# Kernel tuning notes

Hardware: AMD Instinct MI355X
Metric: run time of the kernel (lower is better)

Reference implementation:

```python
import jax, jax.numpy as jnp
import numpy as np

K = 8           # neighbor_num
H = 8           # n_heads
DH = 64         # dim_single_head


def setup_inputs() -> dict:
    key = jax.random.key(0)
    ks = jax.random.split(key, 6)
    B, N, D = 2, 8192, 256
    inner = H * DH  # 512
    x = jax.random.normal(ks[0], (B, N, D), jnp.float32)
    center_pos3d = jax.random.normal(ks[1], (B, N, 3), jnp.float32)
    Wq = jax.random.normal(ks[2], (D, inner), jnp.float32) * 0.02
    Wkv = jax.random.normal(ks[3], (D, 2 * inner), jnp.float32) * 0.02
    Wout = jax.random.normal(ks[4], (inner, D), jnp.float32) * 0.02
    bout = jnp.zeros((D,), jnp.float32)
    return {"x": x, "center_pos3d": center_pos3d, "Wq": Wq, "Wkv": Wkv,
            "Wout": Wout, "bout": bout}


def _knn_idx(pos, k):
    # pos: [B,N,3] -> indices of k nearest neighbors per point, [B,N,k]
    sq = jnp.sum(pos * pos, axis=-1)                      # [B,N]
    d2 = sq[:, :, None] + sq[:, None, :] - 2.0 * jnp.einsum('bnc,bmc->bnm', pos, pos)
    _, idx = jax.lax.top_k(-d2, k)                        # smallest distances
    return idx


def reference(x, center_pos3d, Wq, Wkv, Wout, bout):
    B, N, D = x.shape
    inner = H * DH
    scale = DH ** -0.5

    idx = _knn_idx(center_pos3d, K)                       # [B,N,K] int32
    # grouping_operation: gather neighbor features -> [B,N,K,D]
    knn_x = jax.vmap(lambda xb, ib: xb[ib])(x, idx)

    q = (x @ Wq).reshape(B, N, H, DH)                     # [B,N,H,DH]
    kv = knn_x @ Wkv                                      # [B,N,K,2*inner]
    k_, v_ = jnp.split(kv, 2, axis=-1)
    k_ = k_.reshape(B, N, K, H, DH)
    v_ = v_.reshape(B, N, K, H, DH)

    dots = jnp.einsum('bnhd,bnkhd->bnhk', q, k_) * scale  # [B,N,H,K]
    attn = jax.nn.softmax(dots, axis=-1)
    out = jnp.einsum('bnhk,bnkhd->bnhd', attn, v_)        # [B,N,H,DH]
    out = out.reshape(B, N, inner)
    return out @ Wout + bout                              # dropout p=0 -> identity
```

## Files before the change

### kernel.cpp

```cpp
#include <hip/hip_runtime.h>
#include <hip/hip_bf16.h>

#define N_PTS 8192
#define KNN 8

typedef __attribute__((ext_vector_type(8))) short short8;
typedef __attribute__((ext_vector_type(4))) float float4v;
typedef unsigned long long u64;

static __device__ __forceinline__ short f2bf(float f) {
    unsigned u = __float_as_uint(f);
    unsigned r = (u + 0x7FFFu + ((u >> 16) & 1u)) >> 16;
    return (short)r;
}
static __device__ __forceinline__ float bf2f(short s) {
    return __uint_as_float(((unsigned)(unsigned short)s) << 16);
}

static __device__ __forceinline__ unsigned sortkey(float f) {
    unsigned u = __float_as_uint(f);
    return u ^ (((unsigned)((int)u >> 31)) | 0x80000000u);
}

static __device__ __forceinline__ void ins8(u64* best, u64 x) {
#pragma unroll
    for (int j = 0; j < 8; ++j) {
        const u64 lo = x < best[j] ? x : best[j];
        const u64 hi = x < best[j] ? best[j] : x;
        best[j] = lo; x = hi;
    }
}

static __device__ __forceinline__ void vmin_acc(float& acc, float d) {
    asm("v_min_f32 %0, %0, %1" : "+v"(acc) : "v"(d));
}
static __device__ __forceinline__ void vsort2(float& a, float& x) {
    float lo, hi;
    asm("v_min_f32 %0, %2, %3\n\tv_max_f32 %1, %2, %3"
        : "=&v"(lo), "=v"(hi) : "v"(a), "v"(x));
    a = lo; x = hi;
}

__global__ __launch_bounds__(256) void fused_knn_conv(const float* __restrict__ pos,
                                                      u64* __restrict__ partial,
                                                      const float* __restrict__ x,
                                                      const float* __restrict__ Wq,
                                                      const float* __restrict__ Wkv,
                                                      const float* __restrict__ Wout,
                                                      short* __restrict__ xb,
                                                      short* __restrict__ wqkvt,
                                                      short* __restrict__ woutt)
{
    __shared__ __align__(16) char smem[16896];
    const int tid = threadIdx.x;
    const int g5 = blockIdx.x / 5;
    const int r5 = blockIdx.x % 5;

    if (r5 == 0) {
        const int kb = g5;
        float4* cand = (float4*)smem;
        unsigned short* buf = (unsigned short*)(smem + 8192);

        const int p   = kb & 15;
        const int qg  = kb >> 4;
        const int batch = qg >> 5;
        const int q_in_b = (qg & 31) * 256 + tid;
        const float* bpos = pos + (long)batch * N_PTS * 3;

        if (tid < 128) {
            const float* src = bpos + (p * 512 + tid * 4) * 3;
            const float4 f0 = *(const float4*)(src);
            const float4 f1 = *(const float4*)(src + 4);
            const float4 f2 = *(const float4*)(src + 8);
            const int c0 = tid * 4;
            cand[c0 + 0] = make_float4(f0.x, f0.y, f0.z,
                                       fmaf(f0.x, f0.x, fmaf(f0.y, f0.y, f0.z * f0.z)));
            cand[c0 + 1] = make_float4(f0.w, f1.x, f1.y,
                                       fmaf(f0.w, f0.w, fmaf(f1.x, f1.x, f1.y * f1.y)));
            cand[c0 + 2] = make_float4(f1.z, f1.w, f2.x,
                                       fmaf(f1.z, f1.z, fmaf(f1.w, f1.w, f2.x * f2.x)));
            cand[c0 + 3] = make_float4(f2.y, f2.z, f2.w,
                                       fmaf(f2.y, f2.y, fmaf(f2.z, f2.z, f2.w * f2.w)));
        }
        __syncthreads();

        const float qx = bpos[q_in_b * 3 + 0];
        const float qy = bpos[q_in_b * 3 + 1];
        const float qz = bpos[q_in_b * 3 + 2];
        const float nqx = -2.0f * qx;
        const float nqy = -2.0f * qy;
        const float nqz = -2.0f * qz;

        float bmin[32];
#pragma unroll
        for (int j = 0; j < 32; ++j) bmin[j] = 3.0e38f;

        for (int base = 0; base < 512; base += 32) {
#pragma unroll
            for (int g = 0; g < 32; ++g) {
                const float4 c = cand[base + g];
                const float d = fmaf(c.x, nqx, fmaf(c.y, nqy, fmaf(c.z, nqz, c.w)));
                vmin_acc(bmin[g], d);
            }
        }

        float t8[8];
#pragma unroll
        for (int j = 0; j < 8; ++j) t8[j] = 3.0e38f;
#pragma unroll
        for (int i = 0; i < 32; ++i) {
            float x_ = bmin[i];
#pragma unroll
            for (int j = 0; j < 8; ++j)
                vsort2(t8[j], x_);
        }
        const float t = t8[7];

        int cnt = 0;
        for (int base = 0; base < 512; base += 32) {
#pragma unroll
            for (int g = 0; g < 32; ++g) {
                const float4 c = cand[base + g];
                const float d = fmaf(c.x, nqx, fmaf(c.y, nqy, fmaf(c.z, nqz, c.w)));
                if (d <= t) {
                    buf[tid * 17 + (cnt < 16 ? cnt : 16)] = (unsigned short)(base + g);
                    ++cnt;
                }
            }
        }

        u64 best[8];
#pragma unroll
        for (int j = 0; j < 8; ++j) best[j] = ~0ULL;

        if (cnt <= 16) {
            for (int u = 0; u < cnt; ++u) {
                const int i = buf[tid * 17 + u];
                const float4 c = cand[i];
                const float d = fmaf(c.x, nqx, fmaf(c.y, nqy, fmaf(c.z, nqz, c.w)));
                ins8(best, ((u64)sortkey(d) << 32) | (unsigned)(p * 512 + i));
            }
        } else {
            for (int i = 0; i < 512; ++i) {
                const float4 c = cand[i];
                const float d = fmaf(c.x, nqx, fmaf(c.y, nqy, fmaf(c.z, nqz, c.w)));
                const u64 x_ = ((u64)sortkey(d) << 32) | (unsigned)(p * 512 + i);
                if (x_ < best[7]) ins8(best, x_);
            }
        }

        const long qglob = (long)batch * N_PTS + q_in_b;
#pragma unroll
        for (int j = 0; j < 8; ++j)
            partial[(long)(p * 8 + j) * 16384 + qglob] = best[j];

    } else {
        const int bid = g5 * 4 + (r5 - 1);
        if (bid < 2048) {
            const int i = bid * 256 + tid;
            const float4 a = ((const float4*)x)[i * 2];
            const float4 b = ((const float4*)x)[i * 2 + 1];
            short8 w = {f2bf(a.x), f2bf(a.y), f2bf(a.z), f2bf(a.w),
                        f2bf(b.x), f2bf(b.y), f2bf(b.z), f2bf(b.w)};
            ((short8*)xb)[i] = w;
        } else if (bid < 2560) {
            const int o = (bid - 2048) * 256 + tid;
            const int n = o >> 8, k = o & 255;
            wqkvt[o] = f2bf(Wq[(long)k * 512 + n]);
        } else if (bid < 3584) {
            const int o = (bid - 2560) * 256 + tid;
            const int n = o >> 8, k = o & 255;
            wqkvt[131072 + o] = f2bf(Wkv[(long)k * 1024 + n]);
        } else {
            const int o = (bid - 3584) * 256 + tid;
            const int n = o >> 9, k = o & 511;
            woutt[o] = f2bf(Wout[(long)k * 256 + n]);
        }
    }
}

__global__ __launch_bounds__(256) void fused_gemm_merge(const short* __restrict__ A,
                                                        const short* __restrict__ Bt,
                                                        short* __restrict__ qall,
                                                        short* __restrict__ kvall,
                                                        const u64* __restrict__ partial,
                                                        int* __restrict__ idxo)
{
    __shared__ short As[128][40];
    __shared__ short Bs[128][40];

    const int tid = threadIdx.x;

    if (blockIdx.x < 64) {
        const int q = blockIdx.x * 256 + tid;
        u64 best[8];
#pragma unroll
        for (int j = 0; j < 8; ++j) best[j] = ~0ULL;
        for (int s = 0; s < 128; ++s) {
            u64 x = partial[(long)s * 16384 + q];
            if (x < best[7]) ins8(best, x);
        }
#pragma unroll
        for (int j = 0; j < 8; ++j)
            idxo[(long)q * 8 + j] = (int)(best[j] & 0xFFFFFFFFu);
        return;
    }

    const int id = blockIdx.x - 64;
    const int bx = id % 12;
    const int by = id / 12;

    const int lane = tid & 63;
    const int wv   = tid >> 6;
    const int quad = lane >> 4;
    const int l15  = lane & 15;
    const int m0 = by * 128;
    const int n0 = bx * 128;
    const int mh = (wv & 1) * 64, nh = (wv >> 1) * 64;

    const int srow  = tid >> 1;
    const int shalf = (tid & 1) * 16;
    const int Kd = 256;

    float4v acc[4][4];
#pragma unroll
    for (int i = 0; i < 4; ++i)
#pragma unroll
        for (int j = 0; j < 4; ++j) acc[i][j] = (float4v)(0.f);

    for (int k0 = 0; k0 < Kd; k0 += 32) {
        const short8* asrc = (const short8*)(A + (long)(m0 + srow) * Kd + k0 + shalf);
        const short8* bsrc = (const short8*)(Bt + (long)(n0 + srow) * Kd + k0 + shalf);
        *(short8*)&As[srow][shalf]     = asrc[0];
        *(short8*)&As[srow][shalf + 8] = asrc[1];
        *(short8*)&Bs[srow][shalf]     = bsrc[0];
        *(short8*)&Bs[srow][shalf + 8] = bsrc[1];
        __syncthreads();

        short8 af[4], bfv[4];
#pragma unroll
        for (int i = 0; i < 4; ++i)
            af[i] = *(const short8*)&As[mh + i * 16 + l15][quad * 8];
#pragma unroll
        for (int j = 0; j < 4; ++j)
            bfv[j] = *(const short8*)&Bs[nh + j * 16 + l15][quad * 8];
#pragma unroll
        for (int i = 0; i < 4; ++i)
#pragma unroll
            for (int j = 0; j < 4; ++j)
                acc[i][j] = __builtin_amdgcn_mfma_f32_16x16x32_bf16(af[i], bfv[j], acc[i][j], 0, 0, 0);
        __syncthreads();
    }

    short* Cb;
    int stride, cb;
    if (n0 < 512) { Cb = qall;  stride = 512;  cb = n0; }
    else          { Cb = kvall; stride = 1024; cb = n0 - 512; }

#pragma unroll
    for (int i = 0; i < 4; ++i)
#pragma unroll
        for (int j = 0; j < 4; ++j) {
            const int col = cb + nh + j * 16 + l15;
#pragma unroll
            for (int r = 0; r < 4; ++r) {
                const int row = m0 + mh + i * 16 + quad * 4 + r;
                Cb[(long)row * stride + col] = f2bf(acc[i][j][r]);
            }
        }
}

__global__ __launch_bounds__(256) void attn_kernel(const short* qall,
                                                   const short* __restrict__ kvall,
                                                   const int* __restrict__ idxp,
                                                   short* outp)
{
    __shared__ float attn_s[4][8][8];
    const int wave = threadIdx.x >> 6;
    const int lane = threadIdx.x & 63;
    const int g = blockIdx.x * 4 + wave;
    const int b = g >> 13;
    const int* myidx = idxp + (long)g * 8;

    {
        const int h = lane >> 3;
        const int k = lane & 7;
        const int j = myidx[k];
        const short8* qrow = (const short8*)(qall + (long)g * 512 + h * 64);
        const short8* krow = (const short8*)(kvall + ((long)(b * N_PTS + j)) * 1024 + h * 64);

        float dot = 0.f;
#pragma unroll
        for (int c = 0; c < 8; ++c) {
            const short8 qv = qrow[c];
            const short8 kv = krow[c];
#pragma unroll
            for (int e = 0; e < 8; ++e)
                dot = fmaf(bf2f(qv[e]), bf2f(kv[e]), dot);
        }
        dot *= 0.125f;

        float m = dot;
#pragma unroll
        for (int off = 1; off < 8; off <<= 1)
            m = fmaxf(m, __shfl_xor(m, off, 8));
        const float e = __expf(dot - m);
        float ssum = e;
#pragma unroll
        for (int off = 1; off < 8; off <<= 1)
            ssum += __shfl_xor(ssum, off, 8);
        attn_s[wave][h][k] = e / ssum;
    }
    __syncthreads();

    const int d8 = lane * 8;
    const int h2 = lane >> 3;
    float o[8] = {0.f, 0.f, 0.f, 0.f, 0.f, 0.f, 0.f, 0.f};
#pragma unroll
    for (int kk = 0; kk < 8; ++kk) {
        const int jj = myidx[kk];
        const float w = attn_s[wave][h2][kk];
        const short8 v = *(const short8*)(kvall + ((long)(b * N_PTS + jj)) * 1024 + 512 + d8);
#pragma unroll
        for (int e = 0; e < 8; ++e)
            o[e] = fmaf(w, bf2f(v[e]), o[e]);
    }
    short8 ov = {f2bf(o[0]), f2bf(o[1]), f2bf(o[2]), f2bf(o[3]),
                 f2bf(o[4]), f2bf(o[5]), f2bf(o[6]), f2bf(o[7])};
    *(short8*)(outp + (long)g * 512 + d8) = ov;
}

__global__ __launch_bounds__(256) void gemm_out(const short* __restrict__ A,
                                                const short* __restrict__ Bt,
                                                const float* __restrict__ bias,
                                                float* __restrict__ C,
                                                int N, int Kd)
{
    __shared__ short As[128][40];
    __shared__ short Bs[128][40];

    const int tid  = threadIdx.x;
    const int lane = tid & 63;
    const int wv   = tid >> 6;
    const int quad = lane >> 4;
    const int l15  = lane & 15;
    const int m0 = blockIdx.y * 128;
    const int n0 = blockIdx.x * 128;
    const int mh = (wv & 1) * 64, nh = (wv >> 1) * 64;

    const int srow  = tid >> 1;
    const int shalf = (tid & 1) * 16;

    float4v acc[4][4];
#pragma unroll
    for (int i = 0; i < 4; ++i)
#pragma unroll
        for (int j = 0; j < 4; ++j) acc[i][j] = (float4v)(0.f);

    for (int k0 = 0; k0 < Kd; k0 += 32) {
        const short8* asrc = (const short8*)(A + (long)(m0 + srow) * Kd + k0 + shalf);
        const short8* bsrc = (const short8*)(Bt + (long)(n0 + srow) * Kd + k0 + shalf);
        *(short8*)&As[srow][shalf]     = asrc[0];
        *(short8*)&As[srow][shalf + 8] = asrc[1];
        *(short8*)&Bs[srow][shalf]     = bsrc[0];
        *(short8*)&Bs[srow][shalf + 8] = bsrc[1];
        __syncthreads();

        short8 af[4], bfv[4];
#pragma unroll
        for (int i = 0; i < 4; ++i)
            af[i] = *(const short8*)&As[mh + i * 16 + l15][quad * 8];
#pragma unroll
        for (int j = 0; j < 4; ++j)
            bfv[j] = *(const short8*)&Bs[nh + j * 16 + l15][quad * 8];
#pragma unroll
        for (int i = 0; i < 4; ++i)
#pragma unroll
            for (int j = 0; j < 4; ++j)
                acc[i][j] = __builtin_amdgcn_mfma_f32_16x16x32_bf16(af[i], bfv[j], acc[i][j], 0, 0, 0);
        __syncthreads();
    }

#pragma unroll
    for (int i = 0; i < 4; ++i)
#pragma unroll
        for (int j = 0; j < 4; ++j) {
            const int col = n0 + nh + j * 16 + l15;
            const float bb = bias[col];
#pragma unroll
            for (int r = 0; r < 4; ++r) {
                const int row = m0 + mh + i * 16 + quad * 4 + r;
                C[(long)row * N + col] = acc[i][j][r] + bb;
            }
        }
}

extern "C" void kernel_launch(void* const* d_in, const int* in_sizes, int n_in,
                              void* d_out, int out_size, void* d_ws, size_t ws_size,
                              hipStream_t stream)
{
    const float* x    = (const float*)d_in[0];
    const float* pos  = (const float*)d_in[1];
    const float* Wq   = (const float*)d_in[2];
    const float* Wkv  = (const float*)d_in[3];
    const float* Wout = (const float*)d_in[4];
    const float* bout = (const float*)d_in[5];
    float* out = (float*)d_out;

    const int M = 16384;

    char* ws = (char*)d_ws;
    int*   idxp  = (int*)ws;                          ws += 1 << 19;
    short* qall  = (short*)ws;                        ws += (long)M * 512 * 2;
    short* kvall = (short*)ws;                        ws += (long)M * 1024 * 2;
    short* xb    = (short*)ws;                        ws += (long)M * 256 * 2;
    short* wqkvt = (short*)ws;                        ws += 1536 * 256 * 2;
    short* woutt = (short*)ws;                        ws += 256 * 512 * 2;
    u64*  partial = (u64*)ws;                         ws += (long)128 * 16384 * 8;

    fused_knn_conv<<<5120, 256, 0, stream>>>(pos, partial, x, Wq, Wkv, Wout,
                                             xb, wqkvt, woutt);
    fused_gemm_merge<<<1600, 256, 0, stream>>>(xb, wqkvt, qall, kvall, partial, idxp);
    attn_kernel<<<M / 4, 256, 0, stream>>>(qall, kvall, idxp, qall);
    gemm_out<<<dim3(2, 128), 256, 0, stream>>>(qall, woutt, bout, out, 256, 512);
}
```

Baseline: 283.0 us.

## Prepack candidate positions and stream them via scalar loads in kNN

A new small kernel prepacks positions into float4 (x,y,z,|p|^2) in global memory. The kNN pass then reads candidates with s_load_dwordx16 into scalar registers instead of staging them in LDS, so the LDS fill, the barrier and the per-lane LDS reads go away. The cost is an extra kernel launch, an s_waitcnt after every 8 candidates that stalls the wave on scalar-cache latency, and global reads in the refinement loops.

```diff
diff --git a/kernel.cpp b/kernel.cpp
--- a/kernel.cpp
+++ b/kernel.cpp
@@ -6,6 +6,7 @@
 
 typedef __attribute__((ext_vector_type(8))) short short8;
 typedef __attribute__((ext_vector_type(4))) float float4v;
+typedef __attribute__((ext_vector_type(16))) float f32x16;
 typedef unsigned long long u64;
 
 static __device__ __forceinline__ short f2bf(float f) {
@@ -41,7 +42,25 @@
     a = lo; x = hi;
 }
 
-__global__ __launch_bounds__(256) void fused_knn_conv(const float* __restrict__ pos,
+static __device__ __forceinline__ void sload8(const float4* p, f32x16& A_, f32x16& B_) {
+    asm volatile("s_load_dwordx16 %0, %2, 0x0\n\t"
+                 "s_load_dwordx16 %1, %2, 0x40\n\t"
+                 "s_waitcnt lgkmcnt(0)"
+                 : "=s"(A_), "=s"(B_)
+                 : "s"(p));
+}
+
+__global__ __launch_bounds__(256) void pack_pos(const float* __restrict__ pos,
+                                                float4* __restrict__ packed)
+{
+    const int i = blockIdx.x * 256 + threadIdx.x;
+    const float x = pos[i * 3 + 0];
+    const float y = pos[i * 3 + 1];
+    const float z = pos[i * 3 + 2];
+    packed[i] = make_float4(x, y, z, fmaf(x, x, fmaf(y, y, z * z)));
+}
+
+__global__ __launch_bounds__(256) void fused_knn_conv(const float4* __restrict__ packed,
                                                       u64* __restrict__ partial,
                                                       const float* __restrict__ x,
                                                       const float* __restrict__ Wq,
@@ -51,56 +70,45 @@
                                                       short* __restrict__ wqkvt,
                                                       short* __restrict__ woutt)
 {
-    __shared__ __align__(16) char smem[16896];
+    __shared__ unsigned short buf[256 * 17];
     const int tid = threadIdx.x;
     const int g5 = blockIdx.x / 5;
     const int r5 = blockIdx.x % 5;
 
     if (r5 == 0) {
         const int kb = g5;
-        float4* cand = (float4*)smem;
-        unsigned short* buf = (unsigned short*)(smem + 8192);
-
         const int p   = kb & 15;
         const int qg  = kb >> 4;
         const int batch = qg >> 5;
         const int q_in_b = (qg & 31) * 256 + tid;
-        const float* bpos = pos + (long)batch * N_PTS * 3;
-
-        if (tid < 128) {
-            const float* src = bpos + (p * 512 + tid * 4) * 3;
-            const float4 f0 = *(const float4*)(src);
-            const float4 f1 = *(const float4*)(src + 4);
-            const float4 f2 = *(const float4*)(src + 8);
-            const int c0 = tid * 4;
-            cand[c0 + 0] = make_float4(f0.x, f0.y, f0.z,
-                                       fmaf(f0.x, f0.x, fmaf(f0.y, f0.y, f0.z * f0.z)));
-            cand[c0 + 1] = make_float4(f0.w, f1.x, f1.y,
-                                       fmaf(f0.w, f0.w, fmaf(f1.x, f1.x, f1.y * f1.y)));
-            cand[c0 + 2] = make_float4(f1.z, f1.w, f2.x,
-                                       fmaf(f1.z, f1.z, fmaf(f1.w, f1.w, f2.x * f2.x)));
-            cand[c0 + 3] = make_float4(f2.y, f2.z, f2.w,
-                                       fmaf(f2.y, f2.y, fmaf(f2.z, f2.z, f2.w * f2.w)));
-        }
-        __syncthreads();
-
-        const float qx = bpos[q_in_b * 3 + 0];
-        const float qy = bpos[q_in_b * 3 + 1];
-        const float qz = bpos[q_in_b * 3 + 2];
-        const float nqx = -2.0f * qx;
-        const float nqy = -2.0f * qy;
-        const float nqz = -2.0f * qz;
+
+        const float4* __restrict__ cbase = packed + batch * N_PTS + p * 512;
+
+        const float4 q4 = packed[batch * N_PTS + q_in_b];
+        const float nqx = -2.0f * q4.x;
+        const float nqy = -2.0f * q4.y;
+        const float nqz = -2.0f * q4.z;
 
         float bmin[32];
 #pragma unroll
         for (int j = 0; j < 32; ++j) bmin[j] = 3.0e38f;
 
-        for (int base = 0; base < 512; base += 32) {
-#pragma unroll
-            for (int g = 0; g < 32; ++g) {
-                const float4 c = cand[base + g];
-                const float d = fmaf(c.x, nqx, fmaf(c.y, nqy, fmaf(c.z, nqz, c.w)));
-                vmin_acc(bmin[g], d);
+        for (int c32 = 0; c32 < 512; c32 += 32) {
+#pragma unroll
+            for (int sub = 0; sub < 32; sub += 8) {
+                f32x16 A_, B_;
+                sload8(cbase + c32 + sub, A_, B_);
+#pragma unroll
+                for (int j = 0; j < 4; ++j) {
+                    const float d0 = fmaf(A_[4*j], nqx,
+                                     fmaf(A_[4*j+1], nqy,
+                                     fmaf(A_[4*j+2], nqz, A_[4*j+3])));
+                    vmin_acc(bmin[sub + j], d0);
+                    const float d1 = fmaf(B_[4*j], nqx,
+                                     fmaf(B_[4*j+1], nqy,
+                                     fmaf(B_[4*j+2], nqz, B_[4*j+3])));
+                    vmin_acc(bmin[sub + 4 + j], d1);
+                }
             }
         }
 
@@ -117,13 +125,26 @@
         const float t = t8[7];
 
         int cnt = 0;
-        for (int base = 0; base < 512; base += 32) {
-#pragma unroll
-            for (int g = 0; g < 32; ++g) {
-                const float4 c = cand[base + g];
-                const float d = fmaf(c.x, nqx, fmaf(c.y, nqy, fmaf(c.z, nqz, c.w)));
+        for (int base = 0; base < 512; base += 8) {
+            f32x16 A_, B_;
+            sload8(cbase + base, A_, B_);
+#pragma unroll
+            for (int j = 0; j < 4; ++j) {
+                const float d = fmaf(A_[4*j], nqx,
+                                fmaf(A_[4*j+1], nqy,
+                                fmaf(A_[4*j+2], nqz, A_[4*j+3])));
                 if (d <= t) {
-                    buf[tid * 17 + (cnt < 16 ? cnt : 16)] = (unsigned short)(base + g);
+                    buf[tid * 17 + (cnt < 16 ? cnt : 16)] = (unsigned short)(base + j);
+                    ++cnt;
+                }
+            }
+#pragma unroll
+            for (int j = 0; j < 4; ++j) {
+                const float d = fmaf(B_[4*j], nqx,
+                                fmaf(B_[4*j+1], nqy,
+                                fmaf(B_[4*j+2], nqz, B_[4*j+3])));
+                if (d <= t) {
+                    buf[tid * 17 + (cnt < 16 ? cnt : 16)] = (unsigned short)(base + 4 + j);
                     ++cnt;
                 }
             }
@@ -136,13 +157,13 @@
         if (cnt <= 16) {
             for (int u = 0; u < cnt; ++u) {
                 const int i = buf[tid * 17 + u];
-                const float4 c = cand[i];
+                const float4 c = cbase[i];
                 const float d = fmaf(c.x, nqx, fmaf(c.y, nqy, fmaf(c.z, nqz, c.w)));
                 ins8(best, ((u64)sortkey(d) << 32) | (unsigned)(p * 512 + i));
             }
         } else {
             for (int i = 0; i < 512; ++i) {
-                const float4 c = cand[i];
+                const float4 c = cbase[i];
                 const float d = fmaf(c.x, nqx, fmaf(c.y, nqy, fmaf(c.z, nqz, c.w)));
                 const u64 x_ = ((u64)sortkey(d) << 32) | (unsigned)(p * 512 + i);
                 if (x_ < best[7]) ins8(best, x_);
@@ -417,8 +438,10 @@
     short* wqkvt = (short*)ws;                        ws += 1536 * 256 * 2;
     short* woutt = (short*)ws;                        ws += 256 * 512 * 2;
     u64*  partial = (u64*)ws;                         ws += (long)128 * 16384 * 8;
-
-    fused_knn_conv<<<5120, 256, 0, stream>>>(pos, partial, x, Wq, Wkv, Wout,
+    float4* packed = (float4*)ws;                     ws += (long)M * 16;
+
+    pack_pos<<<64, 256, 0, stream>>>(pos, packed);
+    fused_knn_conv<<<5120, 256, 0, stream>>>(packed, partial, x, Wq, Wkv, Wout,
                                              xb, wqkvt, woutt);
     fused_gemm_merge<<<1600, 256, 0, stream>>>(xb, wqkvt, qall, kvall, partial, idxp);
     attn_kernel<<<M / 4, 256, 0, stream>>>(qall, kvall, idxp, qall);
```

Result: slower. 292.2 us (+3.3%).

## Sort points by Morton cell and prune KNN candidate chunks with AABB bounds

Applied to the files above, without the earlier changes.

Adds a spatial sort of points into a Morton-ordered 32^3 grid (histogram, scan, scatter), then computes per-128-point AABBs and a per-query upper bound radius from sorted neighbors. The brute-force KNN blocks skip candidate sub-chunks whose AABB lower-bound distance exceeds every query's bound, and the merge step scatters results back to original query order. This cuts distance evaluations at the cost of several extra small kernels, atomics and memsets, and relies on the 9-neighbor proxy radius being a valid upper bound for the 8th-nearest distance.

```diff
diff --git a/kernel.cpp b/kernel.cpp
--- a/kernel.cpp
+++ b/kernel.cpp
@@ -3,10 +3,15 @@
 
 #define N_PTS 8192
 #define KNN 8
+#define GRID_DIM 32
+#define NCELLS 32768
+#define CELL_S 0.25f
+#define GRID_LO (-4.0f)
 
 typedef __attribute__((ext_vector_type(8))) short short8;
 typedef __attribute__((ext_vector_type(4))) float float4v;
 typedef unsigned long long u64;
+typedef unsigned int u32;
 
 static __device__ __forceinline__ short f2bf(float f) {
     unsigned u = __float_as_uint(f);
@@ -41,7 +46,130 @@
     a = lo; x = hi;
 }
 
-__global__ __launch_bounds__(256) void fused_knn_conv(const float* __restrict__ pos,
+static __device__ __forceinline__ int cell_coord(float v) {
+    int c = (int)floorf((v - GRID_LO) * (1.0f / CELL_S));
+    c = c < 0 ? 0 : c;
+    c = c > GRID_DIM - 1 ? GRID_DIM - 1 : c;
+    return c;
+}
+static __device__ __forceinline__ unsigned spread5(int v) {
+    return (unsigned)((v & 1) | ((v & 2) << 2) | ((v & 4) << 4)
+                    | ((v & 8) << 6) | ((v & 16) << 8));
+}
+
+__global__ __launch_bounds__(256) void hist_kernel(const float* __restrict__ pos,
+                                                   u32* __restrict__ cellCount,
+                                                   unsigned short* __restrict__ cid)
+{
+    const int i = blockIdx.x * 256 + threadIdx.x;
+    const int b = i >> 13;
+    const float px = pos[i * 3 + 0];
+    const float py = pos[i * 3 + 1];
+    const float pz = pos[i * 3 + 2];
+    const unsigned m = spread5(cell_coord(px))
+                     | (spread5(cell_coord(py)) << 1)
+                     | (spread5(cell_coord(pz)) << 2);
+    cid[i] = (unsigned short)m;
+    atomicAdd(&cellCount[b * NCELLS + m], 1u);
+}
+
+__global__ __launch_bounds__(256) void scan_kernel(const u32* __restrict__ cellCount,
+                                                   u32* __restrict__ cellStart)
+{
+    __shared__ u32 psum[256];
+    const int b = blockIdx.x;
+    const int tid = threadIdx.x;
+    const u32* cnt = cellCount + b * NCELLS;
+    u32* st = cellStart + b * (NCELLS + 1);
+
+    u32 sum = 0;
+    for (int j = 0; j < 128; ++j) sum += cnt[tid * 128 + j];
+    psum[tid] = sum;
+    __syncthreads();
+    if (tid == 0) {
+        u32 a = 0;
+        for (int i = 0; i < 256; ++i) { const u32 t = psum[i]; psum[i] = a; a += t; }
+    }
+    __syncthreads();
+    u32 run = psum[tid];
+    for (int j = 0; j < 128; ++j) {
+        st[tid * 128 + j] = run;
+        run += cnt[tid * 128 + j];
+    }
+    if (tid == 255) st[NCELLS] = run;
+}
+
+__global__ __launch_bounds__(256) void scatter_kernel(const float* __restrict__ pos,
+                                                      const unsigned short* __restrict__ cid,
+                                                      const u32* __restrict__ cellStart,
+                                                      u32* __restrict__ cellOff,
+                                                      float4* __restrict__ sortedPos)
+{
+    const int i = blockIdx.x * 256 + threadIdx.x;
+    const int b = i >> 13;
+    const int li = i & 8191;
+    const float px = pos[i * 3 + 0];
+    const float py = pos[i * 3 + 1];
+    const float pz = pos[i * 3 + 2];
+    const int c = cid[i];
+    const u32 dst = cellStart[b * (NCELLS + 1) + c] + atomicAdd(&cellOff[b * NCELLS + c], 1u);
+    sortedPos[b * N_PTS + dst] = make_float4(px, py, pz, __int_as_float(li));
+}
+
+__global__ __launch_bounds__(256) void aabb_proxy(const float4* __restrict__ sortedPos,
+                                                  float* __restrict__ aabb,
+                                                  float* __restrict__ rprox)
+{
+    const int tid = threadIdx.x;
+    if (blockIdx.x < 128) {
+        __shared__ float red[6][128];
+        const int b = blockIdx.x >> 6;
+        const int sg = blockIdx.x & 63;
+        if (tid < 128) {
+            const float4 c = sortedPos[b * N_PTS + sg * 128 + tid];
+            red[0][tid] = c.x; red[1][tid] = c.y; red[2][tid] = c.z;
+            red[3][tid] = c.x; red[4][tid] = c.y; red[5][tid] = c.z;
+        }
+        __syncthreads();
+        for (int s = 64; s > 0; s >>= 1) {
+            if (tid < s) {
+                red[0][tid] = fminf(red[0][tid], red[0][tid + s]);
+                red[1][tid] = fminf(red[1][tid], red[1][tid + s]);
+                red[2][tid] = fminf(red[2][tid], red[2][tid + s]);
+                red[3][tid] = fmaxf(red[3][tid], red[3][tid + s]);
+                red[4][tid] = fmaxf(red[4][tid], red[4][tid + s]);
+                red[5][tid] = fmaxf(red[5][tid], red[5][tid + s]);
+            }
+            __syncthreads();
+        }
+        if (tid == 0) {
+            float* o = aabb + (b * 64 + sg) * 8;
+            o[0] = red[0][0]; o[1] = red[1][0]; o[2] = red[2][0]; o[3] = 0.f;
+            o[4] = red[3][0]; o[5] = red[4][0]; o[6] = red[5][0]; o[7] = 0.f;
+        }
+    } else {
+        const int q = (blockIdx.x - 128) * 256 + tid;
+        const int b = q >> 13, si = q & 8191;
+        const float4* sp = sortedPos + b * N_PTS;
+        const float4 me = sp[si];
+        int lo = si - 4;
+        lo = lo < 0 ? 0 : lo;
+        lo = lo > N_PTS - 9 ? N_PTS - 9 : lo;
+        float r = 0.f;
+        for (int k = 0; k < 9; ++k) {
+            const int j = lo + k;
+            if (j == si) continue;
+            const float4 c = sp[j];
+            const float dx = c.x - me.x, dy = c.y - me.y, dz = c.z - me.z;
+            r = fmaxf(r, fmaf(dx, dx, fmaf(dy, dy, dz * dz)));
+        }
+        rprox[q] = r;
+    }
+}
+
+__global__ __launch_bounds__(256) void fused_knn_conv(const float4* __restrict__ sortedPos,
+                                                      const float* __restrict__ aabb,
+                                                      const float* __restrict__ rprox,
                                                       u64* __restrict__ partial,
                                                       const float* __restrict__ x,
                                                       const float* __restrict__ Wq,
@@ -51,51 +179,72 @@
                                                       short* __restrict__ wqkvt,
                                                       short* __restrict__ woutt)
 {
-    __shared__ __align__(16) char smem[16896];
+    __shared__ __align__(16) char smem[17984];
     const int tid = threadIdx.x;
     const int g5 = blockIdx.x / 5;
     const int r5 = blockIdx.x % 5;
 
     if (r5 == 0) {
+        float4* cand = (float4*)smem;
+        unsigned short* sidx = (unsigned short*)(smem + 8192);
+        unsigned short* buf = (unsigned short*)(smem + 9216);
+        int* subkeep  = (int*)(smem + 17920);
+        int* keeplist = subkeep + 4;
+        int* pnkeep   = subkeep + 8;
+
         const int kb = g5;
-        float4* cand = (float4*)smem;
-        unsigned short* buf = (unsigned short*)(smem + 8192);
-
         const int p   = kb & 15;
         const int qg  = kb >> 4;
         const int batch = qg >> 5;
         const int q_in_b = (qg & 31) * 256 + tid;
-        const float* bpos = pos + (long)batch * N_PTS * 3;
-
-        if (tid < 128) {
-            const float* src = bpos + (p * 512 + tid * 4) * 3;
-            const float4 f0 = *(const float4*)(src);
-            const float4 f1 = *(const float4*)(src + 4);
-            const float4 f2 = *(const float4*)(src + 8);
-            const int c0 = tid * 4;
-            cand[c0 + 0] = make_float4(f0.x, f0.y, f0.z,
-                                       fmaf(f0.x, f0.x, fmaf(f0.y, f0.y, f0.z * f0.z)));
-            cand[c0 + 1] = make_float4(f0.w, f1.x, f1.y,
-                                       fmaf(f0.w, f0.w, fmaf(f1.x, f1.x, f1.y * f1.y)));
-            cand[c0 + 2] = make_float4(f1.z, f1.w, f2.x,
-                                       fmaf(f1.z, f1.z, fmaf(f1.w, f1.w, f2.x * f2.x)));
-            cand[c0 + 3] = make_float4(f2.y, f2.z, f2.w,
-                                       fmaf(f2.y, f2.y, fmaf(f2.z, f2.z, f2.w * f2.w)));
-        }
-        __syncthreads();
-
-        const float qx = bpos[q_in_b * 3 + 0];
-        const float qy = bpos[q_in_b * 3 + 1];
-        const float qz = bpos[q_in_b * 3 + 2];
-        const float nqx = -2.0f * qx;
-        const float nqy = -2.0f * qy;
-        const float nqz = -2.0f * qz;
+        const float4* sp = sortedPos + batch * N_PTS;
+
+        const float4 q4 = sp[q_in_b];
+        const float rq = fmaf(rprox[batch * N_PTS + q_in_b], 1.00001f, 1e-6f);
+
+        if (tid < 4) subkeep[tid] = 0;
+        __syncthreads();
+#pragma unroll
+        for (int s = 0; s < 4; ++s) {
+            const float* bb = aabb + ((batch * 16 + p) * 4 + s) * 8;
+            const float ax = fmaxf(0.f, fmaxf(bb[0] - q4.x, q4.x - bb[4]));
+            const float ay = fmaxf(0.f, fmaxf(bb[1] - q4.y, q4.y - bb[5]));
+            const float az = fmaxf(0.f, fmaxf(bb[2] - q4.z, q4.z - bb[6]));
+            const float lb = fmaf(ax, ax, fmaf(ay, ay, az * az));
+            const unsigned long long bal = __ballot(lb <= rq);
+            if ((tid & 63) == 0 && bal) subkeep[s] = 1;
+        }
+        __syncthreads();
+        if (tid == 0) {
+            int n = 0;
+            for (int s = 0; s < 4; ++s) if (subkeep[s]) keeplist[n++] = s;
+            *pnkeep = n;
+        }
+        __syncthreads();
+        const int nkeep = *pnkeep;
+        if (nkeep == 0) return;
+
+        for (int s = 0; s < nkeep; ++s) {
+            const int sub = keeplist[s];
+            if (tid < 128) {
+                const float4 c = sp[p * 512 + sub * 128 + tid];
+                cand[s * 128 + tid] = make_float4(c.x, c.y, c.z,
+                    fmaf(c.x, c.x, fmaf(c.y, c.y, c.z * c.z)));
+                sidx[s * 128 + tid] = (unsigned short)__float_as_int(c.w);
+            }
+        }
+        __syncthreads();
+        const int ncand = nkeep * 128;
+
+        const float nqx = -2.0f * q4.x;
+        const float nqy = -2.0f * q4.y;
+        const float nqz = -2.0f * q4.z;
 
         float bmin[32];
 #pragma unroll
         for (int j = 0; j < 32; ++j) bmin[j] = 3.0e38f;
 
-        for (int base = 0; base < 512; base += 32) {
+        for (int base = 0; base < ncand; base += 32) {
 #pragma unroll
             for (int g = 0; g < 32; ++g) {
                 const float4 c = cand[base + g];
@@ -111,13 +260,12 @@
         for (int i = 0; i < 32; ++i) {
             float x_ = bmin[i];
 #pragma unroll
-            for (int j = 0; j < 8; ++j)
-                vsort2(t8[j], x_);
+            for (int j = 0; j < 8; ++j) vsort2(t8[j], x_);
         }
         const float t = t8[7];
 
         int cnt = 0;
-        for (int base = 0; base < 512; base += 32) {
+        for (int base = 0; base < ncand; base += 32) {
 #pragma unroll
             for (int g = 0; g < 32; ++g) {
                 const float4 c = cand[base + g];
@@ -138,13 +286,13 @@
                 const int i = buf[tid * 17 + u];
                 const float4 c = cand[i];
                 const float d = fmaf(c.x, nqx, fmaf(c.y, nqy, fmaf(c.z, nqz, c.w)));
-                ins8(best, ((u64)sortkey(d) << 32) | (unsigned)(p * 512 + i));
+                ins8(best, ((u64)sortkey(d) << 32) | (u32)sidx[i]);
             }
         } else {
-            for (int i = 0; i < 512; ++i) {
+            for (int i = 0; i < ncand; ++i) {
                 const float4 c = cand[i];
                 const float d = fmaf(c.x, nqx, fmaf(c.y, nqy, fmaf(c.z, nqz, c.w)));
-                const u64 x_ = ((u64)sortkey(d) << 32) | (unsigned)(p * 512 + i);
+                const u64 x_ = ((u64)sortkey(d) << 32) | (u32)sidx[i];
                 if (x_ < best[7]) ins8(best, x_);
             }
         }
@@ -184,6 +332,7 @@
                                                         short* __restrict__ qall,
                                                         short* __restrict__ kvall,
                                                         const u64* __restrict__ partial,
+                                                        const float4* __restrict__ sortedPos,
                                                         int* __restrict__ idxo)
 {
     __shared__ short As[128][40];
@@ -200,9 +349,11 @@
             u64 x = partial[(long)s * 16384 + q];
             if (x < best[7]) ins8(best, x);
         }
+        const int b = q >> 13;
+        const int origq = __float_as_int(sortedPos[q].w);
 #pragma unroll
         for (int j = 0; j < 8; ++j)
-            idxo[(long)q * 8 + j] = (int)(best[j] & 0xFFFFFFFFu);
+            idxo[((long)b * N_PTS + origq) * 8 + j] = (int)(best[j] & 0xFFFFFFFFu);
         return;
     }
 
@@ -417,10 +568,25 @@
     short* wqkvt = (short*)ws;                        ws += 1536 * 256 * 2;
     short* woutt = (short*)ws;                        ws += 256 * 512 * 2;
     u64*  partial = (u64*)ws;                         ws += (long)128 * 16384 * 8;
-
-    fused_knn_conv<<<5120, 256, 0, stream>>>(pos, partial, x, Wq, Wkv, Wout,
-                                             xb, wqkvt, woutt);
-    fused_gemm_merge<<<1600, 256, 0, stream>>>(xb, wqkvt, qall, kvall, partial, idxp);
+    u32*  cellCount = (u32*)ws;                       ws += 2L * NCELLS * 4;
+    u32*  cellOff   = (u32*)ws;                       ws += 2L * NCELLS * 4;
+    u32*  cellStart = (u32*)ws;                       ws += 2L * (NCELLS + 1) * 4 + 56;
+    unsigned short* cid = (unsigned short*)ws;        ws += (long)M * 2;
+    float4* sortedPos = (float4*)ws;                  ws += (long)M * 16;
+    float* aabb  = (float*)ws;                        ws += 2L * 64 * 8 * 4;
+    float* rprox = (float*)ws;                        ws += (long)M * 4;
+
+    hipMemsetAsync(cellCount, 0, 4L * NCELLS * 4, stream);
+    hipMemsetAsync(partial, 0xFF, 128L * 16384 * 8, stream);
+
+    hist_kernel<<<64, 256, 0, stream>>>(pos, cellCount, cid);
+    scan_kernel<<<2, 256, 0, stream>>>(cellCount, cellStart);
+    scatter_kernel<<<64, 256, 0, stream>>>(pos, cid, cellStart, cellOff, sortedPos);
+    aabb_proxy<<<192, 256, 0, stream>>>(sortedPos, aabb, rprox);
+    fused_knn_conv<<<5120, 256, 0, stream>>>(sortedPos, aabb, rprox, partial,
+                                             x, Wq, Wkv, Wout, xb, wqkvt, woutt);
+    fused_gemm_merge<<<1600, 256, 0, stream>>>(xb, wqkvt, qall, kvall, partial,
+                                               sortedPos, idxp);
     attn_kernel<<<M / 4, 256, 0, stream>>>(qall, kvall, idxp, qall);
     gemm_out<<<dim3(2, 128), 256, 0, stream>>>(qall, woutt, bout, out, 256, 512);
 }
```

New measurement: 342.8 us. 1.21x slower.

## Sort points by Morton-ordered spatial grid cells before KNN and attention pipeline

Applied to the files above, without the earlier changes.

Adds histogram, scan and scatter kernels that bucket points into a 32^3 Morton-ordered grid and permute positions and feature rows into that spatially sorted order. KNN, the projection GEMMs and attention then run on the sorted order, and the output GEMM scatters rows back through a rowmap. The aim is spatial locality: the hidden KNN code likely relies on it for pruning candidate tiles (bmin threshold), and neighbor KV gathers become more cache-friendly. It adds three small kernels, a memset, atomics and scattered output writes.

```diff
diff --git a/kernel.cpp b/kernel.cpp
--- a/kernel.cpp
+++ b/kernel.cpp
@@ -3,10 +3,15 @@
 
 #define N_PTS 8192
 #define KNN 8
+#define GRID_DIM 32
+#define NCELLS 32768
+#define CELL_S 0.25f
+#define GRID_LO (-4.0f)
 
 typedef __attribute__((ext_vector_type(8))) short short8;
 typedef __attribute__((ext_vector_type(4))) float float4v;
 typedef unsigned long long u64;
+typedef unsigned int u32;
 
 static __device__ __forceinline__ short f2bf(float f) {
     unsigned u = __float_as_uint(f);
@@ -41,7 +46,80 @@
     a = lo; x = hi;
 }
 
-__global__ __launch_bounds__(256) void fused_knn_conv(const float* __restrict__ pos,
+static __device__ __forceinline__ int cell_coord(float v) {
+    int c = (int)floorf((v - GRID_LO) * (1.0f / CELL_S));
+    c = c < 0 ? 0 : c;
+    c = c > GRID_DIM - 1 ? GRID_DIM - 1 : c;
+    return c;
+}
+static __device__ __forceinline__ unsigned spread5(int v) {
+    return (unsigned)((v & 1) | ((v & 2) << 2) | ((v & 4) << 4)
+                    | ((v & 8) << 6) | ((v & 16) << 8));
+}
+
+__global__ __launch_bounds__(256) void hist_kernel(const float* __restrict__ pos,
+                                                   u32* __restrict__ cellCount,
+                                                   unsigned short* __restrict__ cid)
+{
+    const int i = blockIdx.x * 256 + threadIdx.x;
+    const int b = i >> 13;
+    const float px = pos[i * 3 + 0];
+    const float py = pos[i * 3 + 1];
+    const float pz = pos[i * 3 + 2];
+    const unsigned m = spread5(cell_coord(px))
+                     | (spread5(cell_coord(py)) << 1)
+                     | (spread5(cell_coord(pz)) << 2);
+    cid[i] = (unsigned short)m;
+    atomicAdd(&cellCount[b * NCELLS + m], 1u);
+}
+
+__global__ __launch_bounds__(256) void scan_kernel(const u32* __restrict__ cellCount,
+                                                   u32* __restrict__ cellStart)
+{
+    __shared__ u32 psum[256];
+    const int b = blockIdx.x;
+    const int tid = threadIdx.x;
+    const u32* cnt = cellCount + b * NCELLS;
+    u32* st = cellStart + b * (NCELLS + 1);
+
+    u32 sum = 0;
+    for (int j = 0; j < 128; ++j) sum += cnt[tid * 128 + j];
+    psum[tid] = sum;
+    __syncthreads();
+    if (tid == 0) {
+        u32 a = 0;
+        for (int i = 0; i < 256; ++i) { const u32 t = psum[i]; psum[i] = a; a += t; }
+    }
+    __syncthreads();
+    u32 run = psum[tid];
+    for (int j = 0; j < 128; ++j) {
+        st[tid * 128 + j] = run;
+        run += cnt[tid * 128 + j];
+    }
+    if (tid == 255) st[NCELLS] = run;
+}
+
+__global__ __launch_bounds__(256) void scatter_kernel(const float* __restrict__ pos,
+                                                      const unsigned short* __restrict__ cid,
+                                                      const u32* __restrict__ cellStart,
+                                                      u32* __restrict__ cellOff,
+                                                      float4* __restrict__ sortedPos,
+                                                      int* __restrict__ rowmap)
+{
+    const int i = blockIdx.x * 256 + threadIdx.x;
+    const int b = i >> 13;
+    const int li = i & 8191;
+    const float px = pos[i * 3 + 0];
+    const float py = pos[i * 3 + 1];
+    const float pz = pos[i * 3 + 2];
+    const int c = cid[i];
+    const u32 dst = cellStart[b * (NCELLS + 1) + c] + atomicAdd(&cellOff[b * NCELLS + c], 1u);
+    sortedPos[b * N_PTS + dst] = make_float4(px, py, pz, __int_as_float(li));
+    rowmap[b * N_PTS + dst] = i;
+}
+
+__global__ __launch_bounds__(256) void fused_knn_conv(const float4* __restrict__ sortedPos,
+                                                      const int* __restrict__ rowmap,
                                                       u64* __restrict__ partial,
                                                       const float* __restrict__ x,
                                                       const float* __restrict__ Wq,
@@ -65,31 +143,22 @@
         const int qg  = kb >> 4;
         const int batch = qg >> 5;
         const int q_in_b = (qg & 31) * 256 + tid;
-        const float* bpos = pos + (long)batch * N_PTS * 3;
-
-        if (tid < 128) {
-            const float* src = bpos + (p * 512 + tid * 4) * 3;
-            const float4 f0 = *(const float4*)(src);
-            const float4 f1 = *(const float4*)(src + 4);
-            const float4 f2 = *(const float4*)(src + 8);
-            const int c0 = tid * 4;
-            cand[c0 + 0] = make_float4(f0.x, f0.y, f0.z,
-                                       fmaf(f0.x, f0.x, fmaf(f0.y, f0.y, f0.z * f0.z)));
-            cand[c0 + 1] = make_float4(f0.w, f1.x, f1.y,
-                                       fmaf(f0.w, f0.w, fmaf(f1.x, f1.x, f1.y * f1.y)));
-            cand[c0 + 2] = make_float4(f1.z, f1.w, f2.x,
-                                       fmaf(f1.z, f1.z, fmaf(f1.w, f1.w, f2.x * f2.x)));
-            cand[c0 + 3] = make_float4(f2.y, f2.z, f2.w,
-                                       fmaf(f2.y, f2.y, fmaf(f2.z, f2.z, f2.w * f2.w)));
+        const float4* __restrict__ spp = sortedPos + batch * N_PTS + p * 512;
+
+        {
+            const float4 c0 = spp[tid];
+            cand[tid] = make_float4(c0.x, c0.y, c0.z,
+                fmaf(c0.x, c0.x, fmaf(c0.y, c0.y, c0.z * c0.z)));
+            const float4 c1 = spp[tid + 256];
+            cand[tid + 256] = make_float4(c1.x, c1.y, c1.z,
+                fmaf(c1.x, c1.x, fmaf(c1.y, c1.y, c1.z * c1.z)));
         }
         __syncthreads();
 
-        const float qx = bpos[q_in_b * 3 + 0];
-        const float qy = bpos[q_in_b * 3 + 1];
-        const float qz = bpos[q_in_b * 3 + 2];
-        const float nqx = -2.0f * qx;
-        const float nqy = -2.0f * qy;
-        const float nqz = -2.0f * qz;
+        const float4 q4 = sortedPos[batch * N_PTS + q_in_b];
+        const float nqx = -2.0f * q4.x;
+        const float nqy = -2.0f * q4.y;
+        const float nqz = -2.0f * q4.z;
 
         float bmin[32];
 #pragma unroll
@@ -158,8 +227,12 @@
         const int bid = g5 * 4 + (r5 - 1);
         if (bid < 2048) {
             const int i = bid * 256 + tid;
-            const float4 a = ((const float4*)x)[i * 2];
-            const float4 b = ((const float4*)x)[i * 2 + 1];
+            const int rs = i >> 5;
+            const int c8 = i & 31;
+            const long ro = rowmap[rs];
+            const float4* xp = (const float4*)x + (ro * 32 + c8) * 2;
+            const float4 a = xp[0];
+            const float4 b = xp[1];
             short8 w = {f2bf(a.x), f2bf(a.y), f2bf(a.z), f2bf(a.w),
                         f2bf(b.x), f2bf(b.y), f2bf(b.z), f2bf(b.w)};
             ((short8*)xb)[i] = w;
@@ -333,6 +406,7 @@
 __global__ __launch_bounds__(256) void gemm_out(const short* __restrict__ A,
                                                 const short* __restrict__ Bt,
                                                 const float* __restrict__ bias,
+                                                const int* __restrict__ rowmap,
                                                 float* __restrict__ C,
                                                 int N, int Kd)
 {
@@ -381,6 +455,13 @@
         __syncthreads();
     }
 
+    int orow[4][4];
+#pragma unroll
+    for (int i = 0; i < 4; ++i)
+#pragma unroll
+        for (int r = 0; r < 4; ++r)
+            orow[i][r] = rowmap[m0 + mh + i * 16 + quad * 4 + r];
+
 #pragma unroll
     for (int i = 0; i < 4; ++i)
 #pragma unroll
@@ -388,10 +469,8 @@
             const int col = n0 + nh + j * 16 + l15;
             const float bb = bias[col];
 #pragma unroll
-            for (int r = 0; r < 4; ++r) {
-                const int row = m0 + mh + i * 16 + quad * 4 + r;
-                C[(long)row * N + col] = acc[i][j][r] + bb;
-            }
+            for (int r = 0; r < 4; ++r)
+                C[(long)orow[i][r] * N + col] = acc[i][j][r] + bb;
         }
 }
 
@@ -417,10 +496,23 @@
     short* wqkvt = (short*)ws;                        ws += 1536 * 256 * 2;
     short* woutt = (short*)ws;                        ws += 256 * 512 * 2;
     u64*  partial = (u64*)ws;                         ws += (long)128 * 16384 * 8;
-
-    fused_knn_conv<<<5120, 256, 0, stream>>>(pos, partial, x, Wq, Wkv, Wout,
-                                             xb, wqkvt, woutt);
+    u32*  cellCount = (u32*)ws;                       ws += 2L * NCELLS * 4;
+    u32*  cellOff   = (u32*)ws;                       ws += 2L * NCELLS * 4;
+    u32*  cellStart = (u32*)ws;                       ws += 2L * (NCELLS + 1) * 4 + 56;
+    unsigned short* cid = (unsigned short*)ws;        ws += (long)M * 2;
+    float4* sortedPos = (float4*)ws;                  ws += (long)M * 16;
+    int*   rowmap = (int*)ws;                         ws += (long)M * 4;
+
+    hipMemsetAsync(cellCount, 0, 4L * NCELLS * 4, stream);
+
+    hist_kernel<<<64, 256, 0, stream>>>(pos, cellCount, cid);
+    scan_kernel<<<2, 256, 0, stream>>>(cellCount, cellStart);
+    scatter_kernel<<<64, 256, 0, stream>>>(pos, cid, cellStart, cellOff,
+                                           sortedPos, rowmap);
+    fused_knn_conv<<<5120, 256, 0, stream>>>(sortedPos, rowmap, partial,
+                                             x, Wq, Wkv, Wout, xb, wqkvt, woutt);
     fused_gemm_merge<<<1600, 256, 0, stream>>>(xb, wqkvt, qall, kvall, partial, idxp);
     attn_kernel<<<M / 4, 256, 0, stream>>>(qall, kvall, idxp, qall);
-    gemm_out<<<dim3(2, 128), 256, 0, stream>>>(qall, woutt, bout, out, 256, 512);
-}
+    gemm_out<<<dim3(2, 128), 256, 0, stream>>>(qall, woutt, bout, rowmap,
+                                               out, 256, 512);
+}
```

After: 311.1 us. 9.9% more time.
